# Performance work log

Measured on AMD Instinct MI355X. Metric: run time of the kernel, lower is better.

## Reference

```python
import jax, jax.numpy as jnp
import numpy as np

TWO_PI = 2.0 * np.pi


def quat2mat3(q):
    # q: (B,4) (w,x,y,z), normalized internally -> (B,3,3)
    q = q / jnp.linalg.norm(q, axis=-1, keepdims=True)
    w, x, y, z = q[:, 0], q[:, 1], q[:, 2], q[:, 3]
    R = jnp.stack([
        1 - 2 * (y * y + z * z), 2 * (x * y - w * z), 2 * (x * z + w * y),
        2 * (x * y + w * z), 1 - 2 * (x * x + z * z), 2 * (y * z - w * x),
        2 * (x * z - w * y), 2 * (y * z + w * x), 1 - 2 * (x * x + y * y),
    ], axis=-1).reshape(-1, 3, 3)
    return R


def se3(R, t):
    # R: (B,3,3), t: (B,3) -> (B,4,4)
    B = R.shape[0]
    top = jnp.concatenate([R, t[:, :, None]], axis=2)            # (B,3,4)
    bottom = jnp.broadcast_to(jnp.array([[0., 0., 0., 1.]], R.dtype), (B, 1, 4))
    return jnp.concatenate([top, bottom], axis=1)


def mat2quat(R):
    # batched rotation matrix -> quaternion (w,x,y,z), branchless 4-case Shepperd
    R00, R01, R02 = R[:, 0, 0], R[:, 0, 1], R[:, 0, 2]
    R10, R11, R12 = R[:, 1, 0], R[:, 1, 1], R[:, 1, 2]
    R20, R21, R22 = R[:, 2, 0], R[:, 2, 1], R[:, 2, 2]
    tr = R00 + R11 + R22
    t0 = 1.0 + tr
    t1 = 1.0 + R00 - R11 - R22
    t2 = 1.0 - R00 + R11 - R22
    t3 = 1.0 - R00 - R11 + R22
    q0 = jnp.stack([t0, R21 - R12, R02 - R20, R10 - R01], axis=-1)
    q1 = jnp.stack([R21 - R12, t1, R01 + R10, R02 + R20], axis=-1)
    q2 = jnp.stack([R02 - R20, R01 + R10, t2, R12 + R21], axis=-1)
    q3 = jnp.stack([R10 - R01, R02 + R20, R12 + R21, t3], axis=-1)
    qs = jnp.stack([q0, q1, q2, q3], axis=1)   # (B,4,4)
    ts = jnp.stack([t0, t1, t2, t3], axis=1)   # (B,4)
    diag = jnp.stack([R00, R11, R22], axis=1)
    sel = jnp.where(tr > 0, 0, 1 + jnp.argmax(diag, axis=1))
    q = jnp.take_along_axis(qs, sel[:, None, None].astype(jnp.int32).repeat(4, 2), axis=1)[:, 0]
    t = jnp.take_along_axis(ts, sel[:, None].astype(jnp.int32), axis=1)[:, 0]
    return q * (0.5 / jnp.sqrt(jnp.clip(t, 1e-12)))[:, None]


def quat_mul(a, b):
    aw, av = a[:, :1], a[:, 1:]
    bw, bv = b[:, :1], b[:, 1:]
    w = aw * bw - jnp.sum(av * bv, axis=1, keepdims=True)
    v = aw * bv + bw * av + jnp.cross(av, bv)
    return jnp.concatenate([w, v], axis=1)


def quat_distance(q, r):
    r_inv = jnp.concatenate([r[:, :1], -r[:, 1:]], axis=1)  # conjugate (unit quats)
    d = quat_mul(q, r_inv)
    return 2.0 * jnp.arctan2(jnp.linalg.norm(d[:, 1:], axis=1), jnp.abs(d[:, 0]))


def smooth_l1(x, y):
    d = jnp.abs(x - y)
    return jnp.where(d < 1.0, 0.5 * d * d, d - 0.5)


def _rand_se3(key, B):
    kq, kt = jax.random.split(key)
    q = jax.random.normal(kq, (B, 4), jnp.float32)
    R = quat2mat3(q)
    t = jax.random.normal(kt, (B, 3), jnp.float32)
    return se3(R, t)


def setup_inputs() -> dict:
    key = jax.random.key(0)
    B, N = 8, 1_000_000
    k1, k2, k3, k4, k5 = jax.random.split(key, 5)
    return {
        "pred_translation": 0.1 * jax.random.normal(k1, (B, 3), jnp.float32),
        "pred_rotation": jax.random.normal(k2, (B, 4), jnp.float32),
        "pcs": 20.0 * jax.random.normal(k3, (B, N, 3), jnp.float32),
        "gt_T_to_camera": _rand_se3(k4, B),
        "init_T_to_camera": _rand_se3(k5, B),
        "mask": jnp.ones((B, N), jnp.int32),
    }


def reference(pred_translation, pred_rotation, pcs, gt_T_to_camera, init_T_to_camera, mask):
    W_T, W_R, W_PC, W_QN = 1.0, 0.5, 0.5, 0.5
    B = pcs.shape[0]

    # quat norm loss on raw predicted quaternion
    norm_sq = jnp.sum(pred_rotation ** 2, axis=1)
    qn_loss = jnp.mean((norm_sq - 1.0) ** 2)

    # T_pred = trans(t) @ rot(q)  -> (B,4,4)
    T_t = se3(jnp.broadcast_to(jnp.eye(3, dtype=pcs.dtype), (B, 3, 3)), pred_translation)
    T_r = se3(quat2mat3(pred_rotation), jnp.zeros((B, 3), pcs.dtype))
    T_pred = jnp.einsum('bij,bjk->bik', T_t, T_r)

    # T_gt_expected = inv(T_pred) @ init_T
    T_gt_exp = jnp.einsum('bij,bjk->bik', jnp.linalg.inv(T_pred), init_T_to_camera)
    p_t = T_gt_exp[:, :3, 3]
    p_R = T_gt_exp[:, :3, :3]
    g_t = gt_T_to_camera[:, :3, 3]
    g_R = gt_T_to_camera[:, :3, :3]

    # translation: smooth-L1, sum over axes, mean over batch
    t_loss = jnp.mean(jnp.sum(smooth_l1(p_t, g_t), axis=1))

    # PC reprojection: RT_total = inv(gt_T) @ [p_R|p_t]
    T_pred2 = se3(p_R, p_t)
    RT = jnp.einsum('bij,bjk->bik', jnp.linalg.inv(gt_T_to_camera), T_pred2)
    pts = jnp.einsum('bij,bnj->bni', RT[:, :3, :3], pcs) + RT[:, None, :3, 3]
    err = jnp.linalg.norm(pts - pcs, axis=2)               # (B,N)
    mf = mask.astype(pcs.dtype)
    pc_loss = jnp.mean(jnp.sum(err * mf, axis=1) / jnp.sum(mf, axis=1))

    # rotation: quaternion geodesic distance between matrix-derived quats
    r_loss = jnp.mean(quat_distance(mat2quat(p_R), mat2quat(g_R)))

    loss = W_T * t_loss + W_R * r_loss + W_PC * pc_loss + W_QN * qn_loss
    return loss
```

## Files before the change

kernel.cpp:

```cpp
#include <hip/hip_runtime.h>
#include <math.h>

struct Pose {
    float M[9], Tt[3], pR[9], pt[3], gR[9], gt[3], qn;
};

__device__ __forceinline__ float smooth_l1f(float x, float y) {
    float d = fabsf(x - y);
    return d < 1.0f ? 0.5f * d * d : d - 0.5f;
}

__device__ void mat2quat_dev(const float* R, float* q) {
    float R00=R[0],R01=R[1],R02=R[2];
    float R10=R[3],R11=R[4],R12=R[5];
    float R20=R[6],R21=R[7],R22=R[8];
    float tr = R00 + R11 + R22;
    float t;
    if (tr > 0.0f) {
        t = 1.0f + tr;
        q[0]=t; q[1]=R21-R12; q[2]=R02-R20; q[3]=R10-R01;
    } else {
        int sel = 1; float best = R00;
        if (R11 > best) { sel = 2; best = R11; }
        if (R22 > best) { sel = 3; }
        if (sel == 1)      { t = 1.0f+R00-R11-R22; q[0]=R21-R12; q[1]=t; q[2]=R01+R10; q[3]=R02+R20; }
        else if (sel == 2) { t = 1.0f-R00+R11-R22; q[0]=R02-R20; q[1]=R01+R10; q[2]=t; q[3]=R12+R21; }
        else               { t = 1.0f-R00-R11+R22; q[0]=R10-R01; q[1]=R02+R20; q[2]=R12+R21; q[3]=t; }
    }
    float s = 0.5f / sqrtf(fmaxf(t, 1e-12f));
    q[0]*=s; q[1]*=s; q[2]*=s; q[3]*=s;
}

__device__ void compute_pose(int b,
                             const float* __restrict__ pred_t,
                             const float* __restrict__ pred_q,
                             const float* __restrict__ gtT,
                             const float* __restrict__ initT,
                             Pose& P)
{
    float tx=pred_t[b*3+0], ty=pred_t[b*3+1], tz=pred_t[b*3+2];
    float q0=pred_q[b*4+0], q1=pred_q[b*4+1], q2=pred_q[b*4+2], q3=pred_q[b*4+3];
    float nsq = q0*q0+q1*q1+q2*q2+q3*q3;
    P.qn = (nsq-1.0f)*(nsq-1.0f);
    float inv = rsqrtf(nsq);
    float w=q0*inv, x=q1*inv, y=q2*inv, z=q3*inv;
    float R[9];
    R[0]=1.0f-2.0f*(y*y+z*z); R[1]=2.0f*(x*y-w*z);      R[2]=2.0f*(x*z+w*y);
    R[3]=2.0f*(x*y+w*z);      R[4]=1.0f-2.0f*(x*x+z*z); R[5]=2.0f*(y*z-w*x);
    R[6]=2.0f*(x*z-w*y);      R[7]=2.0f*(y*z+w*x);      R[8]=1.0f-2.0f*(x*x+y*y);

    float iR[9], it[3];
    for (int i=0;i<3;i++){
        for (int j=0;j<3;j++){
            iR[i*3+j]=initT[b*16+i*4+j];
            P.gR[i*3+j]=gtT[b*16+i*4+j];
        }
        it[i]=initT[b*16+i*4+3];
        P.gt[i]=gtT[b*16+i*4+3];
    }
    for (int i=0;i<3;i++){
        for (int j=0;j<3;j++)
            P.pR[i*3+j] = R[0+i]*iR[0+j] + R[3+i]*iR[3+j] + R[6+i]*iR[6+j];
        P.pt[i] = R[0+i]*(it[0]-tx) + R[3+i]*(it[1]-ty) + R[6+i]*(it[2]-tz);
    }
    for (int i=0;i<3;i++){
        for (int j=0;j<3;j++)
            P.M[i*3+j] = P.gR[0+i]*P.pR[0+j] + P.gR[3+i]*P.pR[3+j] + P.gR[6+i]*P.pR[6+j];
        P.Tt[i] = P.gR[0+i]*(P.pt[0]-P.gt[0]) + P.gR[3+i]*(P.pt[1]-P.gt[1]) + P.gR[6+i]*(P.pt[2]-P.gt[2]);
    }
    P.M[0]-=1.0f; P.M[4]-=1.0f; P.M[8]-=1.0f;
}

__device__ float scalar_terms(const Pose& P, int B) {
    float t_term = smooth_l1f(P.pt[0],P.gt[0]) + smooth_l1f(P.pt[1],P.gt[1])
                 + smooth_l1f(P.pt[2],P.gt[2]);
    float qp[4], qg[4];
    mat2quat_dev(P.pR,qp); mat2quat_dev(P.gR,qg);
    float dw  = qp[0]*qg[0] + qp[1]*qg[1] + qp[2]*qg[2] + qp[3]*qg[3];
    float cx  = qp[2]*qg[3]-qp[3]*qg[2];
    float cy  = qp[3]*qg[1]-qp[1]*qg[3];
    float cz  = qp[1]*qg[2]-qp[2]*qg[1];
    float dvx = -qp[0]*qg[1] + qg[0]*qp[1] - cx;
    float dvy = -qp[0]*qg[2] + qg[0]*qp[2] - cy;
    float dvz = -qp[0]*qg[3] + qg[0]*qp[3] - cz;
    float r_term = 2.0f*atan2f(sqrtf(dvx*dvx+dvy*dvy+dvz*dvz), fabsf(dw));
    return (1.0f*t_term + 0.5f*r_term + 0.5f*P.qn) / (float)B;
}

#define TP  512
#define F4T 384
#define M4T 128

__global__ __launch_bounds__(256) void pc_fused(const float* __restrict__ pcs,
                                                const int* __restrict__ mask,
                                                const float* __restrict__ pred_t,
                                                const float* __restrict__ pred_q,
                                                const float* __restrict__ gtT,
                                                const float* __restrict__ initT,
                                                float2* __restrict__ partS,
                                                float* __restrict__ scalarS,
                                                int N, int bpb, int chunk, int B)
{
    int b   = blockIdx.x / bpb;
    int blk = blockIdx.x - b*bpb;
    int t   = threadIdx.x;

    __shared__ float sMT[12];
    __shared__ float sP[2][F4T*4];
    __shared__ float sK[2][TP];
    __shared__ float sE[4], sM[4];

    int r0 = blk * chunk;
    if (r0 >= N) {
        if (t==0) partS[blockIdx.x] = make_float2(0.0f, 0.0f);
        return;
    }
    int my_pts = N - r0; if (my_pts > chunk) my_pts = chunk;
    int nt    = (my_pts + TP - 1) / TP;
    int my_f4 = (my_pts * 3) >> 2;
    int my_m4 = my_pts >> 2;

    const float4* pf4 = (const float4*)pcs  + ((size_t)b*N + r0)*3/4;
    const int4*   mi4 = (const int4*)  mask + ((size_t)b*N + r0)/4;

    if (t == 0) {
        Pose P;
        compute_pose(b, pred_t, pred_q, gtT, initT, P);
        #pragma unroll
        for (int k=0;k<9;k++) sMT[k]=P.M[k];
        sMT[9]=P.Tt[0]; sMT[10]=P.Tt[1]; sMT[11]=P.Tt[2];
        if (blk == 0) scalarS[b] = scalar_terms(P, B);
    }

    float4 rA = make_float4(0,0,0,0);
    float4 rB = make_float4(0,0,0,0);
    float4 rM = make_float4(0,0,0,0);

    auto stage = [&](int ti) {
        int fbase = ti * F4T;
        bool full = (ti*TP + TP <= my_pts);
        if (full) {
            rA = pf4[fbase + t];
            if (t < 128) {
                rB = pf4[fbase + 256 + t];
                int4 m = mi4[ti*M4T + t];
                rM = make_float4((float)m.x,(float)m.y,(float)m.z,(float)m.w);
            }
        } else {
            int s0 = fbase + t;
            rA = (s0 < my_f4) ? pf4[s0] : make_float4(0,0,0,0);
            if (t < 128) {
                int s1 = fbase + 256 + t;
                rB = (s1 < my_f4) ? pf4[s1] : make_float4(0,0,0,0);
                int s2 = ti*M4T + t;
                if (s2 < my_m4) {
                    int4 m = mi4[s2];
                    rM = make_float4((float)m.x,(float)m.y,(float)m.z,(float)m.w);
                } else rM = make_float4(0,0,0,0);
            }
        }
    };
    auto wr = [&](int buf) {
        ((float4*)sP[buf])[t] = rA;
        if (t < 128) {
            ((float4*)sP[buf])[256 + t] = rB;
            ((float4*)sK[buf])[t]       = rM;
        }
    };

    stage(0);
    __syncthreads();
    float m00=sMT[0], m01=sMT[1], m02=sMT[2];
    float m10=sMT[3], m11=sMT[4], m12=sMT[5];
    float m20=sMT[6], m21=sMT[7], m22=sMT[8];
    float t0 =sMT[9], t1 =sMT[10], t2 =sMT[11];
    wr(0);
    __syncthreads();

    float esum = 0.0f, msum = 0.0f;
    for (int ti = 0; ti < nt; ti++) {
        int cur = ti & 1;
        if (ti + 1 < nt) stage(ti + 1);
        #pragma unroll
        for (int k = 0; k < 2; k++) {
            int p = t + (k << 8);
            float x = sP[cur][3*p], y = sP[cur][3*p+1], z = sP[cur][3*p+2];
            float mm = sK[cur][p];
            float dx = fmaf(m00,x, fmaf(m01,y, fmaf(m02,z, t0)));
            float dy = fmaf(m10,x, fmaf(m11,y, fmaf(m12,z, t1)));
            float dz = fmaf(m20,x, fmaf(m21,y, fmaf(m22,z, t2)));
            esum = fmaf(mm, sqrtf(fmaf(dx,dx, fmaf(dy,dy, dz*dz))), esum);
            msum += mm;
        }
        if (ti + 1 < nt) wr(cur ^ 1);
        __syncthreads();
    }

    for (int off=32; off>0; off>>=1){
        esum += __shfl_down(esum, off);
        msum += __shfl_down(msum, off);
    }
    int lane = t & 63, wid = t >> 6;
    if (lane==0){ sE[wid]=esum; sM[wid]=msum; }
    __syncthreads();
    if (t==0)
        partS[blockIdx.x] = make_float2(sE[0]+sE[1]+sE[2]+sE[3],
                                        sM[0]+sM[1]+sM[2]+sM[3]);
}

__global__ void finish_kernel(const float2* __restrict__ partS,
                              const float* __restrict__ scalarS,
                              float* __restrict__ out, int B, int bpb)
{
    int t = threadIdx.x;
    int g = t >> 5, sub = t & 31;
    int per = bpb / 32;
    __shared__ double sPC[8];

    float e = 0.0f, m = 0.0f;
    if (g < B) {
        const float2* base = partS + (size_t)g*bpb + sub*per;
        for (int k = 0; k < per; k++) { float2 v = base[k]; e += v.x; m += v.y; }
    }
    for (int off=16; off>0; off>>=1){
        e += __shfl_down(e, off, 32);
        m += __shfl_down(m, off, 32);
    }
    if (sub == 0 && g < B) sPC[g] = (double)e / (double)m;
    __syncthreads();
    if (t == 0) {
        double pc = 0.0; float sc = 0.0f;
        for (int b=0;b<B;b++){ pc += sPC[b]; sc += scalarS[b]; }
        out[0] = sc + 0.5f * (float)(pc / (double)B);
    }
}

extern "C" void kernel_launch(void* const* d_in, const int* in_sizes, int n_in,
                              void* d_out, int out_size, void* d_ws, size_t ws_size,
                              hipStream_t stream)
{
    const float* pred_t = (const float*)d_in[0];
    const float* pred_q = (const float*)d_in[1];
    const float* pcs    = (const float*)d_in[2];
    const float* gtT    = (const float*)d_in[3];
    const float* initT  = (const float*)d_in[4];
    const int*   mask   = (const int*)d_in[5];

    int B = in_sizes[0] / 3;
    int N = in_sizes[2] / (B * 3);

    int bpb   = 256;
    int chunk = (((N + bpb - 1) / bpb) + 3) & ~3;
    int grid  = B * bpb;

    float2* partS   = (float2*)d_ws;
    float*  scalarS = (float*)(partS + grid);
    float*  out     = (float*)d_out;

    pc_fused<<<grid, 256, 0, stream>>>(pcs, mask, pred_t, pred_q, gtT, initT,
                                       partS, scalarS, N, bpb, chunk, B);
    finish_kernel<<<1, 256, 0, stream>>>(partS, scalarS, out, B, bpb);
}
```

Before: 27.82 us.

## Deepen load pipeline with two register stages and keep mask in registers

Doubles the point tile to 1024 points per iteration and keeps two register prefetch sets alternating, so global loads run two tiles ahead. The mask no longer goes through shared memory: each thread reads the int4 mask for its own four consecutive points, and the points come from shared memory as three float4 reads. It also lowers blocks per batch from 256 to 192. The aim is more bytes in flight and fewer shared-memory passes per point, at the cost of more registers and fewer, larger blocks.

```diff
diff --git a/kernel.cpp b/kernel.cpp
--- a/kernel.cpp
+++ b/kernel.cpp
@@ -87,9 +87,8 @@
     return (1.0f*t_term + 0.5f*r_term + 0.5f*P.qn) / (float)B;
 }
 
-#define TP  512
-#define F4T 384
-#define M4T 128
+#define TP  1024
+#define F4T 768
 
 __global__ __launch_bounds__(256) void pc_fused(const float* __restrict__ pcs,
                                                 const int* __restrict__ mask,
@@ -107,9 +106,9 @@
 
     __shared__ float sMT[12];
     __shared__ float sP[2][F4T*4];
-    __shared__ float sK[2][TP];
     __shared__ float sE[4], sM[4];
 
+    float esum = 0.0f, msum = 0.0f;
     int r0 = blk * chunk;
     if (r0 >= N) {
         if (t==0) partS[blockIdx.x] = make_float2(0.0f, 0.0f);
@@ -123,6 +122,49 @@
     const float4* pf4 = (const float4*)pcs  + ((size_t)b*N + r0)*3/4;
     const int4*   mi4 = (const int4*)  mask + ((size_t)b*N + r0)/4;
 
+    float4 a0, b0, c0; int4 m0;
+    float4 a1, b1, c1; int4 m1;
+
+    auto stage0 = [&](int ti) {
+        int fb = ti * F4T;
+        if (ti*TP + TP <= my_pts) {
+            a0 = pf4[fb       + t];
+            b0 = pf4[fb + 256 + t];
+            c0 = pf4[fb + 512 + t];
+            m0 = mi4[ti*256 + t];
+        } else {
+            int s0 = fb + t, s1 = fb + 256 + t, s2 = fb + 512 + t, sm = ti*256 + t;
+            a0 = (s0 < my_f4) ? pf4[s0] : make_float4(0,0,0,0);
+            b0 = (s1 < my_f4) ? pf4[s1] : make_float4(0,0,0,0);
+            c0 = (s2 < my_f4) ? pf4[s2] : make_float4(0,0,0,0);
+            m0 = (sm < my_m4) ? mi4[sm] : make_int4(0,0,0,0);
+        }
+    };
+    auto stage1 = [&](int ti) {
+        int fb = ti * F4T;
+        if (ti*TP + TP <= my_pts) {
+            a1 = pf4[fb       + t];
+            b1 = pf4[fb + 256 + t];
+            c1 = pf4[fb + 512 + t];
+            m1 = mi4[ti*256 + t];
+        } else {
+            int s0 = fb + t, s1 = fb + 256 + t, s2 = fb + 512 + t, sm = ti*256 + t;
+            a1 = (s0 < my_f4) ? pf4[s0] : make_float4(0,0,0,0);
+            b1 = (s1 < my_f4) ? pf4[s1] : make_float4(0,0,0,0);
+            c1 = (s2 < my_f4) ? pf4[s2] : make_float4(0,0,0,0);
+            m1 = (sm < my_m4) ? mi4[sm] : make_int4(0,0,0,0);
+        }
+    };
+    auto wr0 = [&](int buf) {
+        float4* d = (float4*)sP[buf];
+        d[t] = a0; d[t+256] = b0; d[t+512] = c0;
+    };
+    auto wr1 = [&](int buf) {
+        float4* d = (float4*)sP[buf];
+        d[t] = a1; d[t+256] = b1; d[t+512] = c1;
+    };
+
+    stage0(0);
     if (t == 0) {
         Pose P;
         compute_pose(b, pred_t, pred_q, gtT, initT, P);
@@ -131,68 +173,39 @@
         sMT[9]=P.Tt[0]; sMT[10]=P.Tt[1]; sMT[11]=P.Tt[2];
         if (blk == 0) scalarS[b] = scalar_terms(P, B);
     }
-
-    float4 rA = make_float4(0,0,0,0);
-    float4 rB = make_float4(0,0,0,0);
-    float4 rM = make_float4(0,0,0,0);
-
-    auto stage = [&](int ti) {
-        int fbase = ti * F4T;
-        bool full = (ti*TP + TP <= my_pts);
-        if (full) {
-            rA = pf4[fbase + t];
-            if (t < 128) {
-                rB = pf4[fbase + 256 + t];
-                int4 m = mi4[ti*M4T + t];
-                rM = make_float4((float)m.x,(float)m.y,(float)m.z,(float)m.w);
-            }
-        } else {
-            int s0 = fbase + t;
-            rA = (s0 < my_f4) ? pf4[s0] : make_float4(0,0,0,0);
-            if (t < 128) {
-                int s1 = fbase + 256 + t;
-                rB = (s1 < my_f4) ? pf4[s1] : make_float4(0,0,0,0);
-                int s2 = ti*M4T + t;
-                if (s2 < my_m4) {
-                    int4 m = mi4[s2];
-                    rM = make_float4((float)m.x,(float)m.y,(float)m.z,(float)m.w);
-                } else rM = make_float4(0,0,0,0);
-            }
-        }
-    };
-    auto wr = [&](int buf) {
-        ((float4*)sP[buf])[t] = rA;
-        if (t < 128) {
-            ((float4*)sP[buf])[256 + t] = rB;
-            ((float4*)sK[buf])[t]       = rM;
-        }
-    };
-
-    stage(0);
     __syncthreads();
     float m00=sMT[0], m01=sMT[1], m02=sMT[2];
     float m10=sMT[3], m11=sMT[4], m12=sMT[5];
     float m20=sMT[6], m21=sMT[7], m22=sMT[8];
     float t0 =sMT[9], t1 =sMT[10], t2 =sMT[11];
-    wr(0);
-    __syncthreads();
-
-    float esum = 0.0f, msum = 0.0f;
+    wr0(0);
+    if (nt > 1) stage1(1);
+    __syncthreads();
+
     for (int ti = 0; ti < nt; ti++) {
-        int cur = ti & 1;
-        if (ti + 1 < nt) stage(ti + 1);
+        int s = ti & 1;
+        int4 cM;
+        if (s == 0) { cM = m0; if (ti + 2 < nt) stage0(ti + 2); }
+        else        { cM = m1; if (ti + 2 < nt) stage1(ti + 2); }
+
+        const float4* sp4 = (const float4*)sP[s];
+        float4 A = sp4[3*t], C = sp4[3*t+1], D = sp4[3*t+2];
+        float px[4] = {A.x, A.w, C.z, D.y};
+        float py[4] = {A.y, C.x, C.w, D.z};
+        float pz[4] = {A.z, C.y, D.x, D.w};
+        float mf[4] = {(float)cM.x, (float)cM.y, (float)cM.z, (float)cM.w};
         #pragma unroll
-        for (int k = 0; k < 2; k++) {
-            int p = t + (k << 8);
-            float x = sP[cur][3*p], y = sP[cur][3*p+1], z = sP[cur][3*p+2];
-            float mm = sK[cur][p];
-            float dx = fmaf(m00,x, fmaf(m01,y, fmaf(m02,z, t0)));
-            float dy = fmaf(m10,x, fmaf(m11,y, fmaf(m12,z, t1)));
-            float dz = fmaf(m20,x, fmaf(m21,y, fmaf(m22,z, t2)));
-            esum = fmaf(mm, sqrtf(fmaf(dx,dx, fmaf(dy,dy, dz*dz))), esum);
-            msum += mm;
-        }
-        if (ti + 1 < nt) wr(cur ^ 1);
+        for (int j=0;j<4;j++){
+            float dx = fmaf(m00,px[j], fmaf(m01,py[j], fmaf(m02,pz[j], t0)));
+            float dy = fmaf(m10,px[j], fmaf(m11,py[j], fmaf(m12,pz[j], t1)));
+            float dz = fmaf(m20,px[j], fmaf(m21,py[j], fmaf(m22,pz[j], t2)));
+            esum = fmaf(mf[j], sqrtf(fmaf(dx,dx, fmaf(dy,dy, dz*dz))), esum);
+            msum += mf[j];
+        }
+
+        if (ti + 1 < nt) {
+            if (s == 0) wr1(1); else wr0(0);
+        }
         __syncthreads();
     }
 
@@ -249,7 +262,7 @@
     int B = in_sizes[0] / 3;
     int N = in_sizes[2] / (B * 3);
 
-    int bpb   = 256;
+    int bpb   = 192;
     int chunk = (((N + bpb - 1) / bpb) + 3) & ~3;
     int grid  = B * bpb;
 
```

After: 31.22 us. 12.2% more time.
